# Optimization experiments

Measured on AMD Instinct MI355X. Metric: run time of the kernel, lower is better.

## Reference

```python
import jax, jax.numpy as jnp
import numpy as np

EMBED_VOCAB = 16 * 1024 * 1024
EPS = 1e-5


def setup_inputs() -> dict:
    key = jax.random.key(0)
    ks = jax.random.split(key, 16)
    B = 65536
    state = jax.random.randint(ks[0], (B,), 0, 4, dtype=jnp.int32)
    counts = jax.random.randint(ks[1], (B,), 0, 200, dtype=jnp.int32)
    mp = jax.random.randint(ks[2], (B, 7, 7), 0, EMBED_VOCAB, dtype=jnp.int32)
    # learned parameters
    embed_table = jax.random.normal(ks[3], (EMBED_VOCAB, 8), dtype=jnp.float32)
    state_table = jax.random.normal(ks[4], (4, 32), dtype=jnp.float32)
    counts_table = jax.random.normal(ks[5], (200, 16), dtype=jnp.float32)
    d_in = 8 * 49 + 32 + 16  # 440
    W1 = jax.random.normal(ks[6], (256, d_in), dtype=jnp.float32) * (1.0 / np.sqrt(d_in))
    b1 = jnp.zeros((256,), dtype=jnp.float32)
    gamma = jnp.ones((256,), dtype=jnp.float32)
    beta = jnp.zeros((256,), dtype=jnp.float32)
    W2 = jax.random.normal(ks[7], (64, 256), dtype=jnp.float32) * (1.0 / np.sqrt(256))
    b2 = jnp.zeros((64,), dtype=jnp.float32)
    W3 = jax.random.normal(ks[8], (16, 64), dtype=jnp.float32) * (1.0 / np.sqrt(64))
    b3 = jnp.zeros((16,), dtype=jnp.float32)
    W4 = jax.random.normal(ks[9], (1, 16), dtype=jnp.float32) * 0.25
    b4 = jnp.zeros((1,), dtype=jnp.float32)
    return {
        "state": state, "counts": counts, "mp": mp,
        "embed_table": embed_table, "state_table": state_table, "counts_table": counts_table,
        "W1": W1, "b1": b1, "gamma": gamma, "beta": beta,
        "W2": W2, "b2": b2, "W3": W3, "b3": b3, "W4": W4, "b4": b4,
    }


def reference(state, counts, mp, embed_table, state_table, counts_table,
              W1, b1, gamma, beta, W2, b2, W3, b3, W4, b4):
    B = mp.shape[0]
    # gather embeddings
    x = embed_table[jnp.remainder(mp, EMBED_VOCAB)]      # [B,7,7,8]
    x = x.reshape(B, 49 * 8)                              # flatten dims 1..2 then last
    s = state_table[state]                                # [B,32]
    c = counts_table[counts]                              # [B,16]
    h = jnp.concatenate((s, c, x), axis=1)                # [B,440]
    # Linear 440->256
    h = h @ W1.T + b1
    # BatchNorm1d(256), training mode (batch statistics, biased variance)
    mu = jnp.mean(h, axis=0)
    var = jnp.mean((h - mu) ** 2, axis=0)
    h = (h - mu) * jax.lax.rsqrt(var + EPS) * gamma + beta
    # Linear 256->64 + ReLU
    h = jax.nn.relu(h @ W2.T + b2)
    # Linear 64->16 + ReLU
    h = jax.nn.relu(h @ W3.T + b3)
    # Linear 16->1
    out = h @ W4.T + b4                                   # [B,1]
    return out.reshape(B)
```

## Files before the change

### kernel.cpp

```cpp
#include <hip/hip_runtime.h>

typedef __attribute__((ext_vector_type(4))) float f32x4;
typedef __attribute__((ext_vector_type(8))) short bfrag;

#define NCH 256
#define BN_EPS 1e-5f

__device__ __forceinline__ unsigned short cvt_bf16(float f){
  unsigned u = __float_as_uint(f);
  u += 0x7FFFu + ((u >> 16) & 1u);
  return (unsigned short)(u >> 16);
}
__device__ __forceinline__ float bf16tof(unsigned short h){
  return __uint_as_float(((unsigned)h) << 16);
}
__device__ __forceinline__ void split2(const f32x4 va, const f32x4 vb, bfrag& hi, bfrag& lo){
  #pragma unroll
  for (int e = 0; e < 4; ++e){
    unsigned short h0 = cvt_bf16(va[e]);
    hi[e]   = (short)h0;
    lo[e]   = (short)cvt_bf16(va[e] - bf16tof(h0));
    unsigned short h1b = cvt_bf16(vb[e]);
    hi[4+e] = (short)h1b;
    lo[4+e] = (short)cvt_bf16(vb[e] - bf16tof(h1b));
  }
}

#define GLOAD_LDS16(gp, lp) \
  __builtin_amdgcn_global_load_lds((const __attribute__((address_space(1))) unsigned*)(gp), \
                                   (__attribute__((address_space(3))) unsigned*)(lp), 16, 0, 0)

__global__ void k_prep(const float* __restrict__ W1, const float* __restrict__ W2,
                       unsigned short* __restrict__ W1p, unsigned short* __restrict__ W2p){
  int t = blockIdx.x * 256 + threadIdx.x;
  if (t < 14 * 8192){
    int e = t & 7, l = (t >> 3) & 63, c = (t >> 9) & 15, s = t >> 13;
    int chan = c * 16 + (l & 15);
    int k = s * 32 + (l >> 4) * 8 + e;
    float v = (k < 440) ? W1[chan * 440 + k] : 0.f;
    W1p[s * 8192 + c * 512 + l * 8 + e] = cvt_bf16(v);
  }
  if (t < 16384){
    int e = t & 7, l = (t >> 3) & 63, c = (t >> 9) & 3, s = t >> 11;
    int chan = c * 16 + (l & 15);
    int k = s * 32 + (l >> 4) * 8 + e;
    W2p[s * 2048 + c * 512 + l * 8 + e] = cvt_bf16(W2[chan * 256 + k]);
  }
}

__device__ __forceinline__ void stage_w(const char* __restrict__ wsrc, short* smem,
                                        int S, int BUF, int w, int l){
  #pragma unroll
  for (int r = 0; r < 4; ++r)
    GLOAD_LDS16(wsrc + S * 16384 + (w * 4 + r) * 1024 + l * 16,
                (char*)smem + BUF * 16384 + (w * 4 + r) * 1024);
}

__global__ __launch_bounds__(256, 2) void k_gemm1(
    const int* __restrict__ state, const int* __restrict__ counts, const int* __restrict__ mp,
    const float* __restrict__ embed, const float* __restrict__ stab, const float* __restrict__ ctab,
    const unsigned short* __restrict__ W1p, const float* __restrict__ b1,
    unsigned short* __restrict__ h1b, float* __restrict__ gsum)
{
  __shared__ __align__(16) short smem[2 * 8192];
  __shared__ __align__(16) int   mp_lds[6272];
  __shared__ float wsum[4][256];
  __shared__ float wsq[4][256];

  const int tid = threadIdx.x;
  const int w  = tid >> 6;
  const int l  = tid & 63;
  const int lr = l & 15;
  const int g  = l >> 4;
  const int rowbase = blockIdx.x * 128 + w * 32;
  const int arow0 = rowbase + lr;
  const int arow1 = rowbase + 16 + lr;

  const int st0 = state[arow0] * 32, st1 = state[arow1] * 32;
  const int ct0 = counts[arow0] * 16, ct1 = counts[arow1] * 16;
  const char* wsrc = (const char*)W1p;

  {
    const char* mpsrc = (const char*)(mp + (size_t)blockIdx.x * 6272);
    #pragma unroll
    for (int it = 0; it < 7; ++it){
      int idx = it * 256 + tid;
      if (idx < 1568)
        GLOAD_LDS16(mpsrc + idx * 16, (char*)mp_lds + idx * 16);
    }
  }

  f32x4 xva[2][2], xvb[2][2];
  f32x4 acc0[16], acc1[16];
  #pragma unroll
  for (int i = 0; i < 16; ++i){ acc0[i] = (f32x4){0.f,0.f,0.f,0.f}; acc1[i] = acc0[i]; }

  stage_w(wsrc, smem, 0, 0, w, l);
  {
    const float* p0 = stab + st0 + g * 8;
    const float* p1 = stab + st1 + g * 8;
    xva[0][0] = *(const f32x4*)p0;  xvb[0][0] = *(const f32x4*)(p0 + 4);
    xva[0][1] = *(const f32x4*)p1;  xvb[0][1] = *(const f32x4*)(p1 + 4);
  }
  asm volatile("s_waitcnt vmcnt(0)" ::: "memory");
  __builtin_amdgcn_sched_barrier(0);
  __builtin_amdgcn_s_barrier();

  bfrag ahi0, alo0, ahi1, alo1;

  #pragma unroll
  for (int s = 0; s < 14; ++s){
    if (s < 13) stage_w(wsrc, smem, s + 1, (s + 1) & 1, w, l);
    asm volatile("" ::: "memory");
    __builtin_amdgcn_sched_barrier(0);

    {
      f32x4 va0 = xva[s & 1][0], vb0 = xvb[s & 1][0];
      f32x4 va1 = xva[s & 1][1], vb1 = xvb[s & 1][1];
      if (s == 13 && g == 3){
        va0 = (f32x4){0.f,0.f,0.f,0.f}; vb0 = va0; va1 = va0; vb1 = va0;
      }
      split2(va0, vb0, ahi0, alo0);
      split2(va1, vb1, ahi1, alo1);
    }
    if (s < 13){
      const int S = s + 1;
      int m = 4 * S + g - 6;
      m = m < 0 ? 0 : (m > 48 ? 48 : m);
      const float *p0, *p1;
      if (S == 1 && g < 2){
        p0 = ctab + ct0 + g * 8;
        p1 = ctab + ct1 + g * 8;
      } else {
        p0 = embed + ((mp_lds[(w * 32 + lr) * 49 + m]      & 0xFFFFFF) << 3);
        p1 = embed + ((mp_lds[(w * 32 + 16 + lr) * 49 + m] & 0xFFFFFF) << 3);
      }
      xva[S & 1][0] = *(const f32x4*)p0;  xvb[S & 1][0] = *(const f32x4*)(p0 + 4);
      xva[S & 1][1] = *(const f32x4*)p1;  xvb[S & 1][1] = *(const f32x4*)(p1 + 4);
    }

    __builtin_amdgcn_sched_barrier(0);
    __builtin_amdgcn_s_barrier();

    {
      const char* base = (const char*)smem + (s & 1) * 16384 + l * 16;
      #pragma unroll
      for (int c = 0; c < 16; ++c){
        const bfrag bhi = *(const bfrag*)(base + c * 1024);
        acc0[c] = __builtin_amdgcn_mfma_f32_16x16x32_bf16(ahi0, bhi, acc0[c], 0, 0, 0);
        acc0[c] = __builtin_amdgcn_mfma_f32_16x16x32_bf16(alo0, bhi, acc0[c], 0, 0, 0);
        acc1[c] = __builtin_amdgcn_mfma_f32_16x16x32_bf16(ahi1, bhi, acc1[c], 0, 0, 0);
        acc1[c] = __builtin_amdgcn_mfma_f32_16x16x32_bf16(alo1, bhi, acc1[c], 0, 0, 0);
      }
    }

    __builtin_amdgcn_s_barrier();
  }

  #pragma unroll
  for (int c = 0; c < 16; ++c){
    const int j = c * 16 + lr;
    const float bb = b1[j];
    float s = 0.f, q = 0.f;
    #pragma unroll
    for (int e = 0; e < 4; ++e){
      float h = acc0[c][e] + bb;
      s += h; q += h * h;
      h1b[(rowbase + g * 4 + e) * NCH + j] = cvt_bf16(h);
    }
    #pragma unroll
    for (int e = 0; e < 4; ++e){
      float h = acc1[c][e] + bb;
      s += h; q += h * h;
      h1b[(rowbase + 16 + g * 4 + e) * NCH + j] = cvt_bf16(h);
    }
    s += __shfl_xor(s, 16);  s += __shfl_xor(s, 32);
    q += __shfl_xor(q, 16);  q += __shfl_xor(q, 32);
    if (g == 0){ wsum[w][j] = s; wsq[w][j] = q; }
  }
  __syncthreads();
  {
    float s = wsum[0][tid] + wsum[1][tid] + wsum[2][tid] + wsum[3][tid];
    float q = wsq[0][tid]  + wsq[1][tid]  + wsq[2][tid]  + wsq[3][tid];
    atomicAdd(&gsum[tid], s);
    atomicAdd(&gsum[256 + tid], q);
  }
}

__global__ __launch_bounds__(256, 3) void k_tail(
    const unsigned short* __restrict__ h1b, const float* __restrict__ gsum,
    const float* __restrict__ gamma, const float* __restrict__ beta,
    const unsigned short* __restrict__ W2p,
    const float* __restrict__ b2, const float* __restrict__ W3, const float* __restrict__ b3,
    const float* __restrict__ W4, const float* __restrict__ b4,
    float* __restrict__ out)
{
  __shared__ float ssl[512];
  __shared__ __align__(16) short w2s[16384];
  __shared__ float h2l[4][16][65];

  const int tid = threadIdx.x;
  const int w  = tid >> 6;
  const int l  = tid & 63;
  const int lr = l & 15;
  const int g  = l >> 4;
  const int rowbase = blockIdx.x * 64 + w * 16;

  {
    float su = gsum[tid & 255];
    float sq = gsum[256 + (tid & 255)];
    float mu  = su * (1.f / 65536.f);
    float var = sq * (1.f / 65536.f) - mu * mu;
    float sc  = gamma[tid & 255] * rsqrtf(var + BN_EPS);
    ssl[tid & 255]       = sc;
    ssl[256 + (tid & 255)] = beta[tid & 255] - mu * sc;
  }
  #pragma unroll
  for (int it = 0; it < 8; ++it)
    GLOAD_LDS16((const char*)W2p + (it * 256 + tid) * 16, (char*)w2s + (it * 256 + tid) * 16);
  __syncthreads();

  f32x4 acc[4];
  #pragma unroll
  for (int i = 0; i < 4; ++i) acc[i] = (f32x4){0.f, 0.f, 0.f, 0.f};

  #pragma unroll
  for (int s = 0; s < 8; ++s){
    const int kk = s * 32 + g * 8;
    bfrag hv = *(const bfrag*)(h1b + (rowbase + lr) * 256 + kk);
    bfrag ahi, alo;
    #pragma unroll
    for (int e = 0; e < 8; ++e){
      float x = fmaf(bf16tof((unsigned short)hv[e]), ssl[kk + e], ssl[256 + kk + e]);
      unsigned short h0 = cvt_bf16(x);
      ahi[e] = (short)h0;
      alo[e] = (short)cvt_bf16(x - bf16tof(h0));
    }
    const char* base = (const char*)w2s + s * 4096 + l * 16;
    #pragma unroll
    for (int c = 0; c < 4; ++c){
      const bfrag bhi = *(const bfrag*)(base + c * 1024);
      acc[c] = __builtin_amdgcn_mfma_f32_16x16x32_bf16(ahi, bhi, acc[c], 0, 0, 0);
      acc[c] = __builtin_amdgcn_mfma_f32_16x16x32_bf16(alo, bhi, acc[c], 0, 0, 0);
    }
  }

  #pragma unroll
  for (int c = 0; c < 4; ++c){
    int j = c * 16 + lr;
    float bb = b2[j];
    #pragma unroll
    for (int e = 0; e < 4; ++e){
      float h = acc[c][e] + bb;
      h2l[w][g * 4 + e][j] = h > 0.f ? h : 0.f;
    }
  }
  __syncthreads();

  float a3[4];
  #pragma unroll
  for (int t3 = 0; t3 < 4; ++t3) a3[t3] = b3[g * 4 + t3];
  #pragma unroll 4
  for (int k = 0; k < 64; ++k){
    float hv = h2l[w][lr][k];
    #pragma unroll
    for (int t3 = 0; t3 < 4; ++t3) a3[t3] += hv * W3[(g * 4 + t3) * 64 + k];
  }

  float p = 0.f;
  #pragma unroll
  for (int t3 = 0; t3 < 4; ++t3){
    float h = a3[t3] > 0.f ? a3[t3] : 0.f;
    p += h * W4[g * 4 + t3];
  }
  p += __shfl_xor(p, 16);
  p += __shfl_xor(p, 32);
  if (l < 16) out[rowbase + lr] = p + b4[0];
}

extern "C" void kernel_launch(void* const* d_in, const int* in_sizes, int n_in,
                              void* d_out, int out_size, void* d_ws, size_t ws_size,
                              hipStream_t stream){
  const int*   state = (const int*)d_in[0];
  const int*   counts= (const int*)d_in[1];
  const int*   mp    = (const int*)d_in[2];
  const float* embed = (const float*)d_in[3];
  const float* stab  = (const float*)d_in[4];
  const float* ctab  = (const float*)d_in[5];
  const float* W1    = (const float*)d_in[6];
  const float* b1    = (const float*)d_in[7];
  const float* gamma = (const float*)d_in[8];
  const float* beta  = (const float*)d_in[9];
  const float* W2    = (const float*)d_in[10];
  const float* b2    = (const float*)d_in[11];
  const float* W3    = (const float*)d_in[12];
  const float* b3    = (const float*)d_in[13];
  const float* W4    = (const float*)d_in[14];
  const float* b4    = (const float*)d_in[15];
  float* out = (float*)d_out;

  char* ws = (char*)d_ws;
  unsigned short* h1bf = (unsigned short*)(ws);
  float* gsum          = (float*)(ws + 33554432);
  unsigned short* W1p  = (unsigned short*)(ws + 33556480);
  unsigned short* W2p  = (unsigned short*)(ws + 33785856);

  hipMemsetAsync(gsum, 0, 2048, stream);
  k_prep <<<448, 256, 0, stream>>>(W1, W2, W1p, W2p);
  k_gemm1<<<512, 256, 0, stream>>>(state, counts, mp, embed, stab, ctab,
                                   W1p, b1, h1bf, gsum);
  k_tail <<<1024, 256, 0, stream>>>(h1bf, gsum, gamma, beta, W2p,
                                    b2, W3, b3, W4, b4, out);
}
```

Before: 121.0 us.

## Deepen gather prefetch to three stages, fold memset into prep, halve tail grid

The embedding gather in the first GEMM kernel now prefetches two K-steps ahead with a three-slot register ring and explicit vmcnt waits, so random embedding-table loads have more time to land behind the MFMA work. The gsum zeroing moves from a separate memset call into the weight-prep kernel, which removes one launch. The tail kernel now processes 32 rows per wave in two passes over half as many blocks, spreading the W2 LDS staging and BN scale setup over more rows. In exchange the first kernel holds more live registers, which may hurt occupancy, and the hand-written vmcnt counts must match the number of loads actually in flight.

```diff
diff --git a/kernel.cpp b/kernel.cpp
--- a/kernel.cpp
+++ b/kernel.cpp
@@ -31,7 +31,8 @@
                                    (__attribute__((address_space(3))) unsigned*)(lp), 16, 0, 0)
 
 __global__ void k_prep(const float* __restrict__ W1, const float* __restrict__ W2,
-                       unsigned short* __restrict__ W1p, unsigned short* __restrict__ W2p){
+                       unsigned short* __restrict__ W1p, unsigned short* __restrict__ W2p,
+                       float* __restrict__ gsum){
   int t = blockIdx.x * 256 + threadIdx.x;
   if (t < 14 * 8192){
     int e = t & 7, l = (t >> 3) & 63, c = (t >> 9) & 15, s = t >> 13;
@@ -46,14 +47,15 @@
     int k = s * 32 + (l >> 4) * 8 + e;
     W2p[s * 2048 + c * 512 + l * 8 + e] = cvt_bf16(W2[chan * 256 + k]);
   }
-}
-
-__device__ __forceinline__ void stage_w(const char* __restrict__ wsrc, short* smem,
+  if (t < 512) gsum[t] = 0.f;
+}
+
+__device__ __forceinline__ void stage_w(const char* __restrict__ wsrc, char* smem,
                                         int S, int BUF, int w, int l){
   #pragma unroll
   for (int r = 0; r < 4; ++r)
     GLOAD_LDS16(wsrc + S * 16384 + (w * 4 + r) * 1024 + l * 16,
-                (char*)smem + BUF * 16384 + (w * 4 + r) * 1024);
+                smem + BUF * 16384 + (w * 4 + r) * 1024);
 }
 
 __global__ __launch_bounds__(256, 2) void k_gemm1(
@@ -62,8 +64,8 @@
     const unsigned short* __restrict__ W1p, const float* __restrict__ b1,
     unsigned short* __restrict__ h1b, float* __restrict__ gsum)
 {
-  __shared__ __align__(16) short smem[2 * 8192];
-  __shared__ __align__(16) int   mp_lds[6272];
+  __shared__ __align__(16) char smem[2 * 16384];
+  __shared__ __align__(16) int  mp_lds[6272];
   __shared__ float wsum[4][256];
   __shared__ float wsq[4][256];
 
@@ -90,21 +92,34 @@
     }
   }
 
-  f32x4 xva[2][2], xvb[2][2];
+  f32x4 xva[3][2], xvb[3][2];
   f32x4 acc0[16], acc1[16];
   #pragma unroll
   for (int i = 0; i < 16; ++i){ acc0[i] = (f32x4){0.f,0.f,0.f,0.f}; acc1[i] = acc0[i]; }
 
+  #define ISSUE_X(S) do {                                            \
+    const float *p0_, *p1_;                                          \
+    if ((S) == 0){ p0_ = stab + st0 + g * 8; p1_ = stab + st1 + g * 8; } \
+    else if ((S) == 1 && g < 2){                                     \
+      p0_ = ctab + ct0 + g * 8; p1_ = ctab + ct1 + g * 8;            \
+    } else {                                                         \
+      int m_ = 4 * (S) + g - 6;                                      \
+      m_ = m_ < 0 ? 0 : (m_ > 48 ? 48 : m_);                         \
+      p0_ = embed + ((mp_lds[(w * 32 + lr) * 49 + m_]      & 0xFFFFFF) << 3); \
+      p1_ = embed + ((mp_lds[(w * 32 + 16 + lr) * 49 + m_] & 0xFFFFFF) << 3); \
+    }                                                                \
+    xva[(S)%3][0] = *(const f32x4*)p0_;  xvb[(S)%3][0] = *(const f32x4*)(p0_ + 4); \
+    xva[(S)%3][1] = *(const f32x4*)p1_;  xvb[(S)%3][1] = *(const f32x4*)(p1_ + 4); \
+  } while(0)
+
   stage_w(wsrc, smem, 0, 0, w, l);
-  {
-    const float* p0 = stab + st0 + g * 8;
-    const float* p1 = stab + st1 + g * 8;
-    xva[0][0] = *(const f32x4*)p0;  xvb[0][0] = *(const f32x4*)(p0 + 4);
-    xva[0][1] = *(const f32x4*)p1;  xvb[0][1] = *(const f32x4*)(p1 + 4);
-  }
+  ISSUE_X(0);
   asm volatile("s_waitcnt vmcnt(0)" ::: "memory");
   __builtin_amdgcn_sched_barrier(0);
   __builtin_amdgcn_s_barrier();
+  ISSUE_X(1);
+  asm volatile("" ::: "memory");
+  __builtin_amdgcn_sched_barrier(0);
 
   bfrag ahi0, alo0, ahi1, alo1;
 
@@ -115,35 +130,25 @@
     __builtin_amdgcn_sched_barrier(0);
 
     {
-      f32x4 va0 = xva[s & 1][0], vb0 = xvb[s & 1][0];
-      f32x4 va1 = xva[s & 1][1], vb1 = xvb[s & 1][1];
+      f32x4 va0 = xva[s % 3][0], vb0 = xvb[s % 3][0];
+      f32x4 va1 = xva[s % 3][1], vb1 = xvb[s % 3][1];
       if (s == 13 && g == 3){
         va0 = (f32x4){0.f,0.f,0.f,0.f}; vb0 = va0; va1 = va0; vb1 = va0;
       }
       split2(va0, vb0, ahi0, alo0);
       split2(va1, vb1, ahi1, alo1);
     }
-    if (s < 13){
-      const int S = s + 1;
-      int m = 4 * S + g - 6;
-      m = m < 0 ? 0 : (m > 48 ? 48 : m);
-      const float *p0, *p1;
-      if (S == 1 && g < 2){
-        p0 = ctab + ct0 + g * 8;
-        p1 = ctab + ct1 + g * 8;
-      } else {
-        p0 = embed + ((mp_lds[(w * 32 + lr) * 49 + m]      & 0xFFFFFF) << 3);
-        p1 = embed + ((mp_lds[(w * 32 + 16 + lr) * 49 + m] & 0xFFFFFF) << 3);
-      }
-      xva[S & 1][0] = *(const f32x4*)p0;  xvb[S & 1][0] = *(const f32x4*)(p0 + 4);
-      xva[S & 1][1] = *(const f32x4*)p1;  xvb[S & 1][1] = *(const f32x4*)(p1 + 4);
-    }
-
+    if (s < 12) ISSUE_X(s + 2);
+
+    __builtin_amdgcn_sched_barrier(0);
+    if (s <= 11)      asm volatile("s_waitcnt vmcnt(12)" ::: "memory");
+    else if (s == 12) asm volatile("s_waitcnt vmcnt(8)"  ::: "memory");
+    else              asm volatile("s_waitcnt vmcnt(0)"  ::: "memory");
     __builtin_amdgcn_sched_barrier(0);
     __builtin_amdgcn_s_barrier();
 
     {
-      const char* base = (const char*)smem + (s & 1) * 16384 + l * 16;
+      const char* base = smem + (s & 1) * 16384 + l * 16;
       #pragma unroll
       for (int c = 0; c < 16; ++c){
         const bfrag bhi = *(const bfrag*)(base + c * 1024);
@@ -156,6 +161,7 @@
 
     __builtin_amdgcn_s_barrier();
   }
+  #undef ISSUE_X
 
   #pragma unroll
   for (int c = 0; c < 16; ++c){
@@ -204,78 +210,84 @@
   const int l  = tid & 63;
   const int lr = l & 15;
   const int g  = l >> 4;
-  const int rowbase = blockIdx.x * 64 + w * 16;
+  const int rowbase = blockIdx.x * 128 + w * 32;
 
   {
-    float su = gsum[tid & 255];
-    float sq = gsum[256 + (tid & 255)];
+    float su = gsum[tid];
+    float sq = gsum[256 + tid];
     float mu  = su * (1.f / 65536.f);
     float var = sq * (1.f / 65536.f) - mu * mu;
-    float sc  = gamma[tid & 255] * rsqrtf(var + BN_EPS);
-    ssl[tid & 255]       = sc;
-    ssl[256 + (tid & 255)] = beta[tid & 255] - mu * sc;
+    float sc  = gamma[tid] * rsqrtf(var + BN_EPS);
+    ssl[tid]       = sc;
+    ssl[256 + tid] = beta[tid] - mu * sc;
   }
   #pragma unroll
   for (int it = 0; it < 8; ++it)
     GLOAD_LDS16((const char*)W2p + (it * 256 + tid) * 16, (char*)w2s + (it * 256 + tid) * 16);
   __syncthreads();
 
-  f32x4 acc[4];
-  #pragma unroll
-  for (int i = 0; i < 4; ++i) acc[i] = (f32x4){0.f, 0.f, 0.f, 0.f};
-
-  #pragma unroll
-  for (int s = 0; s < 8; ++s){
-    const int kk = s * 32 + g * 8;
-    bfrag hv = *(const bfrag*)(h1b + (rowbase + lr) * 256 + kk);
-    bfrag ahi, alo;
-    #pragma unroll
-    for (int e = 0; e < 8; ++e){
-      float x = fmaf(bf16tof((unsigned short)hv[e]), ssl[kk + e], ssl[256 + kk + e]);
-      unsigned short h0 = cvt_bf16(x);
-      ahi[e] = (short)h0;
-      alo[e] = (short)cvt_bf16(x - bf16tof(h0));
-    }
-    const char* base = (const char*)w2s + s * 4096 + l * 16;
+  const float b4v = b4[0];
+
+  #pragma unroll
+  for (int t = 0; t < 2; ++t){
+    const int rowt = rowbase + t * 16;
+
+    f32x4 acc[4];
+    #pragma unroll
+    for (int i = 0; i < 4; ++i) acc[i] = (f32x4){0.f, 0.f, 0.f, 0.f};
+
+    #pragma unroll
+    for (int s = 0; s < 8; ++s){
+      const int kk = s * 32 + g * 8;
+      bfrag hv = *(const bfrag*)(h1b + (rowt + lr) * 256 + kk);
+      bfrag ahi, alo;
+      #pragma unroll
+      for (int e = 0; e < 8; ++e){
+        float x = fmaf(bf16tof((unsigned short)hv[e]), ssl[kk + e], ssl[256 + kk + e]);
+        unsigned short h0 = cvt_bf16(x);
+        ahi[e] = (short)h0;
+        alo[e] = (short)cvt_bf16(x - bf16tof(h0));
+      }
+      const char* base = (const char*)w2s + s * 4096 + l * 16;
+      #pragma unroll
+      for (int c = 0; c < 4; ++c){
+        const bfrag bhi = *(const bfrag*)(base + c * 1024);
+        acc[c] = __builtin_amdgcn_mfma_f32_16x16x32_bf16(ahi, bhi, acc[c], 0, 0, 0);
+        acc[c] = __builtin_amdgcn_mfma_f32_16x16x32_bf16(alo, bhi, acc[c], 0, 0, 0);
+      }
+    }
+
     #pragma unroll
     for (int c = 0; c < 4; ++c){
-      const bfrag bhi = *(const bfrag*)(base + c * 1024);
-      acc[c] = __builtin_amdgcn_mfma_f32_16x16x32_bf16(ahi, bhi, acc[c], 0, 0, 0);
-      acc[c] = __builtin_amdgcn_mfma_f32_16x16x32_bf16(alo, bhi, acc[c], 0, 0, 0);
-    }
-  }
-
-  #pragma unroll
-  for (int c = 0; c < 4; ++c){
-    int j = c * 16 + lr;
-    float bb = b2[j];
-    #pragma unroll
-    for (int e = 0; e < 4; ++e){
-      float h = acc[c][e] + bb;
-      h2l[w][g * 4 + e][j] = h > 0.f ? h : 0.f;
-    }
-  }
-  __syncthreads();
-
-  float a3[4];
-  #pragma unroll
-  for (int t3 = 0; t3 < 4; ++t3) a3[t3] = b3[g * 4 + t3];
-  #pragma unroll 4
-  for (int k = 0; k < 64; ++k){
-    float hv = h2l[w][lr][k];
-    #pragma unroll
-    for (int t3 = 0; t3 < 4; ++t3) a3[t3] += hv * W3[(g * 4 + t3) * 64 + k];
-  }
-
-  float p = 0.f;
-  #pragma unroll
-  for (int t3 = 0; t3 < 4; ++t3){
-    float h = a3[t3] > 0.f ? a3[t3] : 0.f;
-    p += h * W4[g * 4 + t3];
-  }
-  p += __shfl_xor(p, 16);
-  p += __shfl_xor(p, 32);
-  if (l < 16) out[rowbase + lr] = p + b4[0];
+      int j = c * 16 + lr;
+      float bb = b2[j];
+      #pragma unroll
+      for (int e = 0; e < 4; ++e){
+        float h = acc[c][e] + bb;
+        h2l[w][g * 4 + e][j] = h > 0.f ? h : 0.f;
+      }
+    }
+
+    float a3[4];
+    #pragma unroll
+    for (int t3 = 0; t3 < 4; ++t3) a3[t3] = b3[g * 4 + t3];
+    #pragma unroll 4
+    for (int k = 0; k < 64; ++k){
+      float hv = h2l[w][lr][k];
+      #pragma unroll
+      for (int t3 = 0; t3 < 4; ++t3) a3[t3] += hv * W3[(g * 4 + t3) * 64 + k];
+    }
+
+    float p = 0.f;
+    #pragma unroll
+    for (int t3 = 0; t3 < 4; ++t3){
+      float h = a3[t3] > 0.f ? a3[t3] : 0.f;
+      p += h * W4[g * 4 + t3];
+    }
+    p += __shfl_xor(p, 16);
+    p += __shfl_xor(p, 32);
+    if (l < 16) out[rowt + lr] = p + b4v;
+  }
 }
 
 extern "C" void kernel_launch(void* const* d_in, const int* in_sizes, int n_in,
@@ -302,13 +314,12 @@
   char* ws = (char*)d_ws;
   unsigned short* h1bf = (unsigned short*)(ws);
   float* gsum          = (float*)(ws + 33554432);
-  unsigned short* W1p  = (unsigned short*)(ws + 33556480);
-  unsigned short* W2p  = (unsigned short*)(ws + 33785856);
-
-  hipMemsetAsync(gsum, 0, 2048, stream);
-  k_prep <<<448, 256, 0, stream>>>(W1, W2, W1p, W2p);
+  unsigned short* W1p  = (unsigned short*)(ws + 33558528);
+  unsigned short* W2p  = (unsigned short*)(ws + 33787904);
+
+  k_prep <<<448, 256, 0, stream>>>(W1, W2, W1p, W2p, gsum);
   k_gemm1<<<512, 256, 0, stream>>>(state, counts, mp, embed, stab, ctab,
                                    W1p, b1, h1bf, gsum);
-  k_tail <<<1024, 256, 0, stream>>>(h1bf, gsum, gamma, beta, W2p,
-                                    b2, W3, b3, W4, b4, out);
-}
+  k_tail <<<512, 256, 0, stream>>>(h1bf, gsum, gamma, beta, W2p,
+                                   b2, W3, b3, W4, b4, out);
+}
```

Result: faster. 117.4 us, median of 2 (-2.9%).
